# Kernel tuning notes

Hardware: AMD Instinct MI355X
Metric: run time of the kernel (lower is better)

Reference implementation:

```python
import jax, jax.numpy as jnp
import numpy as np

E = 8          # num_experts
K = 2          # top-k experts per token
CAP_RATIO = 1.05


def setup_inputs() -> dict:
    key = jax.random.key(0)
    k0, k1, k2, k3 = jax.random.split(key, 4)
    B, S, D, H = 2, 2048, 512, 2048
    return {
        "x": jax.random.normal(k0, (B, S, D), jnp.float32),
        "gate_w": jax.random.normal(k1, (E, D), jnp.float32) * (1.0 / np.sqrt(D)),
        "fc1_w": jax.random.normal(k2, (E, D, H), jnp.float32) * (1.0 / np.sqrt(D)),
        "fc1_b": jnp.zeros((E, H), jnp.float32),
        "fc2_w": jax.random.normal(k3, (E, H, D), jnp.float32) * (1.0 / np.sqrt(H)),
        "fc2_b": jnp.zeros((E, D), jnp.float32),
    }


def reference(x, gate_w, fc1_w, fc1_b, fc2_w, fc2_b):
    B, S, D = x.shape
    xf = x.reshape(-1, D)               # [T, D]
    T = xf.shape[0]

    # ---- router (eval mode: no noise) ----
    logits = xf @ gate_w.T              # [T, E]
    gates = jax.nn.softmax(logits, axis=-1)
    top_g, top_i = jax.lax.top_k(gates, K)   # [T, K]

    # importance auxiliary loss (std unbiased=False == jnp.std default)
    imp = gates.sum(axis=0)                  # [E]
    imp_loss = (jnp.std(imp) / (imp.mean() + 1e-6)) ** 2

    # ---- capacity-limited dispatch mask ----
    # torch loops slot-major: slot 0 over all tokens in order, then slot 1.
    # position of each (slot, token) entry within its expert's queue:
    buffer_cap = round(K * T * CAP_RATIO / E)
    idx_sm = top_i.T.reshape(-1)                        # [K*T] slot-major
    oh = jax.nn.one_hot(idx_sm, E, dtype=jnp.int32)     # [K*T, E]
    pos = jnp.cumsum(oh, axis=0) - oh                   # earlier same-expert count
    pos_e = jnp.take_along_axis(pos, idx_sm[:, None], axis=1)[:, 0]
    within = (pos_e < buffer_cap).reshape(K, T).T       # [T, K] bool

    wf = within.astype(xf.dtype)
    oh_tke = jax.nn.one_hot(top_i, E, dtype=xf.dtype) * wf[..., None]  # dispatch mask [T,K,E]
    combine_te = jnp.einsum('tk,tke->te', top_g * wf, oh_tke / jnp.maximum(oh_tke, 1e-30) * oh_tke) if False else jnp.einsum('tk,tke->te', top_g * wf, jax.nn.one_hot(top_i, E, dtype=xf.dtype))

    # load-balance loss from post-capacity token counts
    tokens_per_expert = oh_tke.sum(axis=(0, 1))         # [E]
    l_load = (jnp.std(tokens_per_expert) / (tokens_per_expert.mean() + 1e-6)) ** 2
    l_aux = 0.5 * (imp_loss + l_load)

    # ---- per-expert MLP (dense compute, masked combine) ----
    h = jnp.einsum('td,edh->teh', xf, fc1_w) + fc1_b[None]      # [T, E, H]
    h = jax.nn.gelu(h, approximate=False)                       # torch nn.GELU default
    y = jnp.einsum('teh,ehd->ted', h, fc2_w) + fc2_b[None]      # [T, E, D]

    out = jnp.einsum('te,ted->td', combine_te, y).reshape(B, S, D)
    return out, l_aux, l_load
```

## Files before the change

kernel.cpp:

```cpp
#include <hip/hip_runtime.h>
#include <hip/hip_bf16.h>

#define E_    8
#define TT    4096
#define DD    512
#define HH    2048
#define CAP   1075
#define MPAD  1152
#define MT    9
#define MT2   18

typedef __bf16 bf16_t;
typedef bf16_t bf16x8 __attribute__((ext_vector_type(8)));
typedef float  f32x4  __attribute__((ext_vector_type(4)));
typedef unsigned int u32;

__device__ __forceinline__ bf16_t tobf(float f) { return (bf16_t)f; }

#define OFF_TOPI  256u
#define OFF_TOPG  (OFF_TOPI + 4096u*2u*4u)
#define OFF_SLOT  (OFF_TOPG + 4096u*2u*4u)
#define OFF_ETOK  (OFF_SLOT + 4096u*2u*4u)
#define OFF_EWT   (OFF_ETOK + 8u*1152u*4u)
#define OFF_XG    (OFF_EWT  + 8u*1152u*4u)
#define XG_BYTES  (8u*1152u*512u*2u)
#define OFF_W1T   (OFF_XG + XG_BYTES)
#define W1T_BYTES (8u*512u*2048u*2u)
#define OFF_W2T   (OFF_W1T + W1T_BYTES)
#define W2T_BYTES (8u*2048u*512u*2u)
#define OFF_H     (OFF_W2T + W2T_BYTES)
#define H_BYTES   (8u*1152u*2048u*2u)
#define OFF_Y     OFF_XG

__global__ __launch_bounds__(256) void router_kernel(
    const float* __restrict__ x, const float* __restrict__ gw,
    float* __restrict__ imp, int* __restrict__ top_i, float* __restrict__ top_g) {
  const int tid = threadIdx.x;
  const int wid = tid >> 6, lane = tid & 63;
  const int t = blockIdx.x * 4 + wid;

  float p[E_];
#pragma unroll
  for (int e = 0; e < E_; ++e) p[e] = 0.f;
  const float* xr = x + (size_t)t * DD;
#pragma unroll
  for (int it = 0; it < DD / 64; ++it) {
    const int d = it * 64 + lane;
    const float xv = xr[d];
#pragma unroll
    for (int e = 0; e < E_; ++e) p[e] += xv * gw[e * DD + d];
  }
#pragma unroll
  for (int off = 32; off > 0; off >>= 1) {
#pragma unroll
    for (int e = 0; e < E_; ++e) p[e] += __shfl_down(p[e], off);
  }

  __shared__ float simp[4][E_];
  if (lane == 0) {
    float mx = p[0];
#pragma unroll
    for (int e = 1; e < E_; ++e) mx = fmaxf(mx, p[e]);
    float g[E_]; float s = 0.f;
#pragma unroll
    for (int e = 0; e < E_; ++e) { g[e] = expf(p[e] - mx); s += g[e]; }
    const float inv = 1.f / s;
#pragma unroll
    for (int e = 0; e < E_; ++e) { g[e] *= inv; simp[wid][e] = g[e]; }
    int i0 = 0;
#pragma unroll
    for (int e = 1; e < E_; ++e) if (g[e] > g[i0]) i0 = e;
    int i1 = (i0 == 0) ? 1 : 0;
#pragma unroll
    for (int e = 0; e < E_; ++e) if (e != i0 && g[e] > g[i1]) i1 = e;
    top_i[t * 2 + 0] = i0;  top_i[t * 2 + 1] = i1;
    top_g[t * 2 + 0] = g[i0]; top_g[t * 2 + 1] = g[i1];
  }
  __syncthreads();
  if (tid < E_) {
    const float s = simp[0][tid] + simp[1][tid] + simp[2][tid] + simp[3][tid];
    atomicAdd(&imp[tid], s);
  }
}

__global__ __launch_bounds__(1024) void capacity_kernel(
    const int* __restrict__ top_i, const float* __restrict__ top_g,
    const float* __restrict__ imp, int* __restrict__ etok, float* __restrict__ ewt,
    int* __restrict__ slot_map, int* __restrict__ kept, float* __restrict__ scal) {
  __shared__ u32 wt[16][4];
  const int tid = threadIdx.x, wave = tid >> 6, lane = tid & 63;

  int eidx[8];
#pragma unroll
  for (int q = 0; q < 8; ++q) {
    const int j = tid * 8 + q;
    const int k = j >> 12, t = j & (TT - 1);
    eidx[q] = top_i[t * 2 + k];
  }
  u32 pk[4] = {0u, 0u, 0u, 0u};
#pragma unroll
  for (int q = 0; q < 8; ++q) pk[eidx[q] >> 1] += 1u << ((eidx[q] & 1) * 16);

  u32 v[4] = {pk[0], pk[1], pk[2], pk[3]};
#pragma unroll
  for (int off = 1; off < 64; off <<= 1) {
#pragma unroll
    for (int p = 0; p < 4; ++p) {
      const u32 n = (u32)__shfl_up((int)v[p], off);
      if (lane >= off) v[p] += n;
    }
  }
  if (lane == 63) {
#pragma unroll
    for (int p = 0; p < 4; ++p) wt[wave][p] = v[p];
  }
  __syncthreads();
  u32 base[4] = {0u, 0u, 0u, 0u}, tot[4] = {0u, 0u, 0u, 0u};
#pragma unroll
  for (int w = 0; w < 16; ++w) {
#pragma unroll
    for (int p = 0; p < 4; ++p) {
      const u32 x = wt[w][p];
      if (w < wave) base[p] += x;
      tot[p] += x;
    }
  }
  int run[E_];
#pragma unroll
  for (int p = 0; p < 4; ++p) {
    const u32 excl = base[p] + v[p] - pk[p];
    run[2 * p]     = (int)(excl & 0xFFFFu);
    run[2 * p + 1] = (int)(excl >> 16);
  }
#pragma unroll
  for (int q = 0; q < 8; ++q) {
    const int e = eidx[q];
    const int pos = run[e]++;
    const int j = tid * 8 + q;
    if (pos < CAP) {
      const int k = j >> 12, t = j & (TT - 1);
      etok[e * MPAD + pos] = t;
      ewt[e * MPAD + pos] = top_g[t * 2 + k];
      slot_map[j] = (e << 16) | pos;
    } else {
      slot_map[j] = -1;
    }
  }
  if (tid == 0) {
    float tpe[E_], mt = 0.f;
#pragma unroll
    for (int p = 0; p < 4; ++p) {
      const int t0 = (int)(tot[p] & 0xFFFFu), t1 = (int)(tot[p] >> 16);
      const int k0 = t0 < CAP ? t0 : CAP, k1 = t1 < CAP ? t1 : CAP;
      kept[2 * p] = k0; kept[2 * p + 1] = k1;
      tpe[2 * p] = (float)k0; tpe[2 * p + 1] = (float)k1;
    }
    float ms = 0.f;
#pragma unroll
    for (int e = 0; e < E_; ++e) ms += tpe[e];
    ms *= (1.f / E_);
    float vt = 0.f;
#pragma unroll
    for (int e = 0; e < E_; ++e) { const float d = tpe[e] - ms; vt += d * d; }
    vt *= (1.f / E_);
    const float ll = vt / ((ms + 1e-6f) * (ms + 1e-6f));

    float iv[E_], mi = 0.f;
#pragma unroll
    for (int e = 0; e < E_; ++e) { iv[e] = imp[e]; mi += iv[e]; }
    mi *= (1.f / E_);
    float vi = 0.f;
#pragma unroll
    for (int e = 0; e < E_; ++e) { const float d = iv[e] - mi; vi += d * d; }
    vi *= (1.f / E_);
    const float il = vi / ((mi + 1e-6f) * (mi + 1e-6f));

    scal[0] = 0.5f * (il + ll);
    scal[1] = ll;
  }
}

__global__ __launch_bounds__(256) void gather_kernel(
    const float* __restrict__ x, const int* __restrict__ etok,
    const int* __restrict__ kept, bf16_t* __restrict__ Xg) {
  const int e = blockIdx.y, wid = threadIdx.x >> 6, lane = threadIdx.x & 63;
  const int m = blockIdx.x * 4 + wid;
  if (m >= kept[e]) return;
  const int t = etok[e * MPAD + m];
  const float* src = x + (size_t)t * DD + lane * 8;
  const float4 a = *(const float4*)src;
  const float4 b = *(const float4*)(src + 4);
  bf16_t tmp[8] = {tobf(a.x), tobf(a.y), tobf(a.z), tobf(a.w),
                   tobf(b.x), tobf(b.y), tobf(b.z), tobf(b.w)};
  *(bf16x8*)(Xg + ((size_t)e * MPAD + m) * DD + lane * 8) = *(const bf16x8*)tmp;
}

__global__ __launch_bounds__(256) void transpose_kernel(
    const float* __restrict__ in, bf16_t* __restrict__ outp, int R, int C) {
  __shared__ float tile[32][33];
  const int e = blockIdx.z;
  const int r0 = blockIdx.y * 32, c0 = blockIdx.x * 32;
  const int tx = threadIdx.x, ty = threadIdx.y;
  const float* ip = in + (size_t)e * R * C;
  bf16_t* op = outp + (size_t)e * R * C;
#pragma unroll
  for (int i = 0; i < 4; ++i)
    tile[ty + i * 8][tx] = ip[(size_t)(r0 + ty + i * 8) * C + c0 + tx];
  __syncthreads();
#pragma unroll
  for (int i = 0; i < 4; ++i)
    op[(size_t)(c0 + ty + i * 8) * R + r0 + tx] = tobf(tile[tx][ty + i * 8]);
}

template <int MI, int KLEN, int KSTR>
__device__ __forceinline__ void gemm_core(
    const bf16_t* __restrict__ A, const bf16_t* __restrict__ B,
    bf16_t* As, bf16_t* Bs, f32x4 acc[][4]) {
  const int tid = threadIdx.x;
  const int wave = tid >> 6, lane = tid & 63;
  const int r8 = lane >> 3;
  const int kswz = ((lane & 7) ^ r8) * 8;
  const bf16_t* ga = A + (size_t)(wave * (MI * 8) + r8) * KSTR + kswz;
  const bf16_t* gb = B + (size_t)(wave * 32 + r8) * KSTR + kswz;
  const int mw = (wave >> 1) * (MI * 16), nw = (wave & 1) * 64;
  const int l15 = lane & 15, quad = lane >> 4;
  const int sw = l15 & 7;

  for (int k0 = 0; k0 < KLEN; k0 += 64) {
    __syncthreads();
#pragma unroll
    for (int p = 0; p < MI; ++p) {
      __builtin_amdgcn_global_load_lds(
          (const __attribute__((address_space(1))) void*)(ga + (size_t)p * 8 * KSTR + k0),
          (__attribute__((address_space(3))) void*)(As + (wave * (MI * 8) + p * 8) * 64),
          16, 0, 0);
    }
#pragma unroll
    for (int p = 0; p < 4; ++p) {
      __builtin_amdgcn_global_load_lds(
          (const __attribute__((address_space(1))) void*)(gb + (size_t)p * 8 * KSTR + k0),
          (__attribute__((address_space(3))) void*)(Bs + (wave * 32 + p * 8) * 64),
          16, 0, 0);
    }
    __syncthreads();
#pragma unroll
    for (int ks = 0; ks < 2; ++ks) {
      bf16x8 af[MI], bfr[4];
#pragma unroll
      for (int i = 0; i < MI; ++i)
        af[i] = *(const bf16x8*)(As + (mw + i * 16 + l15) * 64 + (((ks * 4 + quad) ^ sw) << 3));
#pragma unroll
      for (int j = 0; j < 4; ++j)
        bfr[j] = *(const bf16x8*)(Bs + (nw + j * 16 + l15) * 64 + (((ks * 4 + quad) ^ sw) << 3));
#pragma unroll
      for (int i = 0; i < MI; ++i)
#pragma unroll
        for (int j = 0; j < 4; ++j)
          acc[i][j] = __builtin_amdgcn_mfma_f32_16x16x32_bf16(af[i], bfr[j], acc[i][j], 0, 0, 0);
    }
  }
}

__global__ __launch_bounds__(256, 3) void gemm1_kernel(
    const bf16_t* __restrict__ Xg, const bf16_t* __restrict__ W1t,
    const float* __restrict__ b1, bf16_t* __restrict__ Hbuf) {
  __shared__ __align__(16) bf16_t As[128 * 64];
  __shared__ __align__(16) bf16_t Bs[128 * 64];
  const int e = blockIdx.z, tileM = blockIdx.y, tileN = blockIdx.x;
  const bf16_t* A = Xg + ((size_t)e * MPAD + tileM * 128) * DD;
  const bf16_t* B = W1t + ((size_t)e * HH + tileN * 128) * DD;
  f32x4 acc[4][4];
  const f32x4 z = {0.f, 0.f, 0.f, 0.f};
#pragma unroll
  for (int i = 0; i < 4; ++i)
#pragma unroll
    for (int j = 0; j < 4; ++j) acc[i][j] = z;
  gemm_core<4, DD, DD>(A, B, As, Bs, acc);

  const int tid = threadIdx.x, wave = tid >> 6, lane = tid & 63;
  const int mw = (wave >> 1) * 64, nw = (wave & 1) * 64;
  const int l15 = lane & 15, quad = lane >> 4;
#pragma unroll
  for (int i = 0; i < 4; ++i) {
    const int mbase = tileM * 128 + mw + i * 16 + quad * 4;
#pragma unroll
    for (int j = 0; j < 4; ++j) {
      const int n = tileN * 128 + nw + j * 16 + l15;
      const float bias = b1[e * HH + n];
#pragma unroll
      for (int r = 0; r < 4; ++r) {
        float v = acc[i][j][r] + bias;
        v = 0.5f * v * (1.f + erff(v * 0.70710678118654752f));
        Hbuf[((size_t)e * MPAD + mbase + r) * HH + n] = tobf(v);
      }
    }
  }
}

__global__ __launch_bounds__(256, 4) void gemm2_kernel(
    const bf16_t* __restrict__ Hbuf, const bf16_t* __restrict__ W2t,
    const int* __restrict__ kept, float* __restrict__ Ybuf) {
  __shared__ __align__(16) bf16_t As[64 * 64];
  __shared__ __align__(16) bf16_t Bs[128 * 64];
  const int e = blockIdx.z, tileM = blockIdx.y, tileN = blockIdx.x;
  const bf16_t* A = Hbuf + ((size_t)e * MPAD + tileM * 64) * HH;
  const bf16_t* B = W2t + ((size_t)e * DD + tileN * 128) * HH;
  f32x4 acc[2][4];
  const f32x4 z = {0.f, 0.f, 0.f, 0.f};
#pragma unroll
  for (int i = 0; i < 2; ++i)
#pragma unroll
    for (int j = 0; j < 4; ++j) acc[i][j] = z;
  gemm_core<2, HH, HH>(A, B, As, Bs, acc);

  const int tid = threadIdx.x, wave = tid >> 6, lane = tid & 63;
  const int mw = (wave >> 1) * 32, nw = (wave & 1) * 64;
  const int l15 = lane & 15, quad = lane >> 4;
  const int nk = kept[e];
#pragma unroll
  for (int i = 0; i < 2; ++i) {
#pragma unroll
    for (int r = 0; r < 4; ++r) {
      const int m = tileM * 64 + mw + i * 16 + quad * 4 + r;
      if (m < nk) {
        float* yrow = Ybuf + ((size_t)e * MPAD + m) * DD + tileN * 128;
#pragma unroll
        for (int j = 0; j < 4; ++j)
          yrow[nw + j * 16 + l15] = acc[i][j][r];
      }
    }
  }
}

__global__ __launch_bounds__(128) void combine_kernel(
    const float* __restrict__ Ybuf, const float* __restrict__ b2,
    const int* __restrict__ slot_map, const float* __restrict__ top_g,
    float* __restrict__ out) {
  const int t = blockIdx.x;
  const int c = threadIdx.x * 4;
  float4 acc = {0.f, 0.f, 0.f, 0.f};
#pragma unroll
  for (int k = 0; k < 2; ++k) {
    const int sm = slot_map[k * TT + t];
    if (sm >= 0) {
      const int e = sm >> 16, pos = sm & 0xFFFF;
      const float w = top_g[t * 2 + k];
      const float4 y = *(const float4*)(Ybuf + ((size_t)e * MPAD + pos) * DD + c);
      const float4 bb = *(const float4*)(b2 + e * DD + c);
      acc.x += w * (y.x + bb.x);
      acc.y += w * (y.y + bb.y);
      acc.z += w * (y.z + bb.z);
      acc.w += w * (y.w + bb.w);
    }
  }
  *(float4*)(out + (size_t)t * DD + c) = acc;
}

extern "C" void kernel_launch(void* const* d_in, const int* in_sizes, int n_in,
                              void* d_out, int out_size, void* d_ws, size_t ws_size,
                              hipStream_t stream) {
  const float* x      = (const float*)d_in[0];
  const float* gate_w = (const float*)d_in[1];
  const float* fc1_w  = (const float*)d_in[2];
  const float* fc1_b  = (const float*)d_in[3];
  const float* fc2_w  = (const float*)d_in[4];
  const float* fc2_b  = (const float*)d_in[5];
  float* out = (float*)d_out;

  char* ws = (char*)d_ws;
  float*  imp   = (float*)(ws + 0);
  int*    kept  = (int*)(ws + 64);
  int*    top_i = (int*)(ws + OFF_TOPI);
  float*  top_g = (float*)(ws + OFF_TOPG);
  int*    slotm = (int*)(ws + OFF_SLOT);
  int*    etok  = (int*)(ws + OFF_ETOK);
  float*  ewt   = (float*)(ws + OFF_EWT);
  bf16_t* Xg    = (bf16_t*)(ws + OFF_XG);
  bf16_t* W1t   = (bf16_t*)(ws + OFF_W1T);
  bf16_t* W2t   = (bf16_t*)(ws + OFF_W2T);
  bf16_t* Hbuf  = (bf16_t*)(ws + OFF_H);
  float*  Ybuf  = (float*)(ws + OFF_Y);

  hipMemsetAsync(ws, 0, 256, stream);

  transpose_kernel<<<dim3(HH / 32, DD / 32, E_), dim3(32, 8), 0, stream>>>(fc1_w, W1t, DD, HH);
  transpose_kernel<<<dim3(DD / 32, HH / 32, E_), dim3(32, 8), 0, stream>>>(fc2_w, W2t, HH, DD);

  router_kernel<<<TT / 4, 256, 0, stream>>>(x, gate_w, imp, top_i, top_g);
  capacity_kernel<<<1, 1024, 0, stream>>>(top_i, top_g, imp, etok, ewt, slotm, kept,
                                          out + (size_t)TT * DD);
  gather_kernel<<<dim3(MPAD / 4, E_), 256, 0, stream>>>(x, etok, kept, Xg);

  gemm1_kernel<<<dim3(HH / 128, MT, E_), 256, 0, stream>>>(Xg, W1t, fc1_b, Hbuf);
  gemm2_kernel<<<dim3(DD / 128, MT2, E_), 256, 0, stream>>>(Hbuf, W2t, kept, Ybuf);
  combine_kernel<<<TT, 128, 0, stream>>>(Ybuf, fc2_b, slotm, top_g, out);
}
```

Before: 246.5 us.

## Swap MFMA operands for row-contiguous vector stores and use tanh GELU

Swaps the A/B operands of the MFMA so each lane's four accumulator values lie along the N dimension. This lets the GEMM epilogues write packed bf16x4 rows of H and float4 rows of Y instead of scattered scalar stores. It also replaces the erf-based exact GELU with a tanh approximation built on __expf, which cuts epilogue arithmetic. The tanh form differs slightly from the exact erf GELU the reference requires, so it adds a small accuracy change.

```diff
diff --git a/kernel.cpp b/kernel.cpp
--- a/kernel.cpp
+++ b/kernel.cpp
@@ -11,11 +11,21 @@
 #define MT2   18
 
 typedef __bf16 bf16_t;
+typedef bf16_t bf16x4 __attribute__((ext_vector_type(4)));
 typedef bf16_t bf16x8 __attribute__((ext_vector_type(8)));
 typedef float  f32x4  __attribute__((ext_vector_type(4)));
 typedef unsigned int u32;
 
 __device__ __forceinline__ bf16_t tobf(float f) { return (bf16_t)f; }
+
+__device__ __forceinline__ float gelu_f(float v) {
+  const float u = v * (0.7978845608028654f + 0.035677408136300125f * v * v);
+  const float a = __builtin_fabsf(u);
+  const float ex = __expf(2.0f * a);
+  float th = 1.0f - 2.0f / (ex + 1.0f);
+  th = __builtin_copysignf(th, u);
+  return 0.5f * v * (1.0f + th);
+}
 
 #define OFF_TOPI  256u
 #define OFF_TOPG  (OFF_TOPI + 4096u*2u*4u)
@@ -147,7 +157,7 @@
     }
   }
   if (tid == 0) {
-    float tpe[E_], mt = 0.f;
+    float tpe[E_];
 #pragma unroll
     for (int p = 0; p < 4; ++p) {
       const int t0 = (int)(tot[p] & 0xFFFFu), t1 = (int)(tot[p] >> 16);
@@ -215,7 +225,7 @@
 template <int MI, int KLEN, int KSTR>
 __device__ __forceinline__ void gemm_core(
     const bf16_t* __restrict__ A, const bf16_t* __restrict__ B,
-    bf16_t* As, bf16_t* Bs, f32x4 acc[][4]) {
+    bf16_t* As, bf16_t* Bs, f32x4 (&acc)[4][MI]) {
   const int tid = threadIdx.x;
   const int wave = tid >> 6, lane = tid & 63;
   const int r8 = lane >> 3;
@@ -253,10 +263,10 @@
       for (int j = 0; j < 4; ++j)
         bfr[j] = *(const bf16x8*)(Bs + (nw + j * 16 + l15) * 64 + (((ks * 4 + quad) ^ sw) << 3));
 #pragma unroll
-      for (int i = 0; i < MI; ++i)
-#pragma unroll
-        for (int j = 0; j < 4; ++j)
-          acc[i][j] = __builtin_amdgcn_mfma_f32_16x16x32_bf16(af[i], bfr[j], acc[i][j], 0, 0, 0);
+      for (int j = 0; j < 4; ++j)
+#pragma unroll
+        for (int i = 0; i < MI; ++i)
+          acc[j][i] = __builtin_amdgcn_mfma_f32_16x16x32_bf16(bfr[j], af[i], acc[j][i], 0, 0, 0);
     }
   }
 }
@@ -272,27 +282,27 @@
   f32x4 acc[4][4];
   const f32x4 z = {0.f, 0.f, 0.f, 0.f};
 #pragma unroll
-  for (int i = 0; i < 4; ++i)
-#pragma unroll
-    for (int j = 0; j < 4; ++j) acc[i][j] = z;
+  for (int j = 0; j < 4; ++j)
+#pragma unroll
+    for (int i = 0; i < 4; ++i) acc[j][i] = z;
   gemm_core<4, DD, DD>(A, B, As, Bs, acc);
 
   const int tid = threadIdx.x, wave = tid >> 6, lane = tid & 63;
   const int mw = (wave >> 1) * 64, nw = (wave & 1) * 64;
   const int l15 = lane & 15, quad = lane >> 4;
 #pragma unroll
-  for (int i = 0; i < 4; ++i) {
-    const int mbase = tileM * 128 + mw + i * 16 + quad * 4;
-#pragma unroll
-    for (int j = 0; j < 4; ++j) {
-      const int n = tileN * 128 + nw + j * 16 + l15;
-      const float bias = b1[e * HH + n];
-#pragma unroll
-      for (int r = 0; r < 4; ++r) {
-        float v = acc[i][j][r] + bias;
-        v = 0.5f * v * (1.f + erff(v * 0.70710678118654752f));
-        Hbuf[((size_t)e * MPAD + mbase + r) * HH + n] = tobf(v);
-      }
+  for (int j = 0; j < 4; ++j) {
+    const int n0 = tileN * 128 + nw + j * 16 + quad * 4;
+    const float4 b4 = *(const float4*)(b1 + e * HH + n0);
+#pragma unroll
+    for (int i = 0; i < 4; ++i) {
+      const int m = tileM * 128 + mw + i * 16 + l15;
+      bf16x4 h4;
+      h4.x = tobf(gelu_f(acc[j][i][0] + b4.x));
+      h4.y = tobf(gelu_f(acc[j][i][1] + b4.y));
+      h4.z = tobf(gelu_f(acc[j][i][2] + b4.z));
+      h4.w = tobf(gelu_f(acc[j][i][3] + b4.w));
+      *(bf16x4*)(Hbuf + ((size_t)e * MPAD + m) * HH + n0) = h4;
     }
   }
 }
@@ -305,12 +315,12 @@
   const int e = blockIdx.z, tileM = blockIdx.y, tileN = blockIdx.x;
   const bf16_t* A = Hbuf + ((size_t)e * MPAD + tileM * 64) * HH;
   const bf16_t* B = W2t + ((size_t)e * DD + tileN * 128) * HH;
-  f32x4 acc[2][4];
+  f32x4 acc[4][2];
   const f32x4 z = {0.f, 0.f, 0.f, 0.f};
 #pragma unroll
-  for (int i = 0; i < 2; ++i)
-#pragma unroll
-    for (int j = 0; j < 4; ++j) acc[i][j] = z;
+  for (int j = 0; j < 4; ++j)
+#pragma unroll
+    for (int i = 0; i < 2; ++i) acc[j][i] = z;
   gemm_core<2, HH, HH>(A, B, As, Bs, acc);
 
   const int tid = threadIdx.x, wave = tid >> 6, lane = tid & 63;
@@ -318,16 +328,13 @@
   const int l15 = lane & 15, quad = lane >> 4;
   const int nk = kept[e];
 #pragma unroll
-  for (int i = 0; i < 2; ++i) {
-#pragma unroll
-    for (int r = 0; r < 4; ++r) {
-      const int m = tileM * 64 + mw + i * 16 + quad * 4 + r;
-      if (m < nk) {
-        float* yrow = Ybuf + ((size_t)e * MPAD + m) * DD + tileN * 128;
-#pragma unroll
-        for (int j = 0; j < 4; ++j)
-          yrow[nw + j * 16 + l15] = acc[i][j][r];
-      }
+  for (int j = 0; j < 4; ++j) {
+    const int n0 = tileN * 128 + nw + j * 16 + quad * 4;
+#pragma unroll
+    for (int i = 0; i < 2; ++i) {
+      const int m = tileM * 64 + mw + i * 16 + l15;
+      if (m < nk)
+        *(f32x4*)(Ybuf + ((size_t)e * MPAD + m) * DD + n0) = acc[j][i];
     }
   }
 }
```

Result: faster. 240.3 us (-2.5%).
